# Kernel tuning notes

Hardware: AMD Instinct MI355X
Metric: run time of the kernel (lower is better)

The kernel has to match this reference:

```python
import jax, jax.numpy as jnp
import numpy as np

B, C_IN, C_OUT = 4, 64, 64
Z = H = W = 64
MZ = MH = MW = 16
R = 16


def setup_inputs() -> dict:
    key = jax.random.key(0)
    ks = jax.random.split(key, 12)
    p = lambda k, s: jax.random.normal(k, s, jnp.float32) * 0.02
    return {
        "x": jax.random.normal(ks[0], (B, C_IN, Z, H, W), jnp.float32),
        "U_in": p(ks[1], (C_IN, R)),
        "U_out": p(ks[2], (C_OUT, R)),
        "U_z": p(ks[3], (MZ, R)),
        "U_h": p(ks[4], (MH, R)),
        "U_w": p(ks[5], (MW, R)),
        "U_z2": p(ks[6], (MZ, R)),
        "U_h2": p(ks[7], (MH, R)),
        "core_r": p(ks[8], (R, R, R, R, R)),
        "core_i": p(ks[9], (R, R, R, R, R)),
        "core2_r": p(ks[10], (R, R, R, R, R)),
        "core2_i": p(ks[11], (R, R, R, R, R)),
    }


def _reconstruct(U_in, U_out, Uz, Uh, Uw, core):
    # Original: einsum('ir,or,zr,hr,wr,abcde->iozwh', ..., core).
    # core's a..e indices are summed independently of the shared r index,
    # so the weight equals the CP outer product scaled by core.sum().
    c = jnp.complex64
    w = jnp.einsum('ir,or,zr,hr,wr->iozwh',
                   U_in.astype(c), U_out.astype(c), Uz.astype(c),
                   Uh.astype(c), Uw.astype(c))
    return w * jnp.sum(core)  # (in, out, mz, mw, mh)


def reference(x, U_in, U_out, U_z, U_h, U_w, U_z2, U_h2,
              core_r, core_i, core2_r, core2_i):
    mz, mh, mw = U_z.shape[0], U_h.shape[0], U_w.shape[0]
    b, _, z, h, w = x.shape
    core = core_r + 1j * core_i
    core2 = core2_r + 1j * core2_i

    x_ft = jnp.fft.rfftn(x, axes=(-3, -2, -1))  # (B, Cin, Z, H, W//2+1) c64
    w1 = _reconstruct(U_in, U_out, U_z, U_h, U_w, core)
    w2 = _reconstruct(U_in, U_out, U_z2, U_h2, U_w, core2)

    lo = jnp.einsum('bixyz,ioxyz->boxyz', x_ft[:, :, :mz, :mh, :mw], w1)
    hi = jnp.einsum('bixyz,ioxyz->boxyz', x_ft[:, :, -mz:, :mh, :mw], w2)

    out_ft = jnp.zeros((b, U_out.shape[0], z, h, w // 2 + 1), jnp.complex64)
    out_ft = out_ft.at[:, :, :mz, :mh, :mw].set(lo)
    out_ft = out_ft.at[:, :, -mz:, :mh, :mw].set(hi)

    return jnp.fft.irfftn(out_ft, s=(z, h, w), axes=(-3, -2, -1)).astype(jnp.float32)
```

## Files before the change

kernel.cpp:

```cpp
#include <hip/hip_runtime.h>

#define TWOPI 6.28318530717958647692f

typedef float fvec4 __attribute__((ext_vector_type(4)));

constexpr float COSQ[17] = {
  1.0f, 0.995184727f, 0.980785280f, 0.956940336f, 0.923879533f,
  0.881921264f, 0.831469612f, 0.773010453f, 0.707106781f,
  0.634393284f, 0.555570233f, 0.471396737f, 0.382683432f,
  0.290284677f, 0.195090322f, 0.098017140f, 0.0f
};
__host__ __device__ constexpr float cos64f(int k) {
  k &= 63;
  return (k <= 16) ? COSQ[k] : (k < 32) ? -COSQ[32 - k]
       : (k <= 48) ? -COSQ[k - 32] : COSQ[64 - k];
}
__host__ __device__ constexpr float sin64f(int k) { return cos64f(k + 48); }


__global__ __launch_bounds__(256) void k_fwd_wh_core(
    const float* __restrict__ x, float2* __restrict__ A2,
    const float* __restrict__ a0, const float* __restrict__ a1,
    const float* __restrict__ a2, const float* __restrict__ a3,
    float* __restrict__ partial) {
  __shared__ float2 T[4][64][16];
  if (blockIdx.x < 256) {
    float* red = (float*)T;
    int bx = blockIdx.x & 63, by = blockIdx.x >> 6;
    const float* p = by == 0 ? a0 : by == 1 ? a1 : by == 2 ? a2 : a3;
    const fvec4* p4 = (const fvec4*)p;
    float s = 0.f;
    int base = bx * 4096 + threadIdx.x;
    #pragma unroll
    for (int i = 0; i < 16; ++i) {
      fvec4 v = __builtin_nontemporal_load(&p4[base + i * 256]);
      s += (v.x + v.y) + (v.z + v.w);
    }
    red[threadIdx.x] = s;
    __syncthreads();
    for (int off = 128; off; off >>= 1) {
      if (threadIdx.x < off) red[threadIdx.x] += red[threadIdx.x + off];
      __syncthreads();
    }
    if (threadIdx.x == 0) partial[by * 64 + bx] = red[0];
    return;
  }
  int wave = threadIdx.x >> 6, lane = threadIdx.x & 63;
  int plane = (blockIdx.x - 256) * 4 + wave;
  const float* xp = x + (size_t)plane * 4096 + lane;
  float cre[16], cim[16];
  {
    float x0 = xp[0], x32 = xp[32 * 64];
    #pragma unroll
    for (int hf = 0; hf < 16; ++hf) {
      cre[hf] = x0 + ((hf & 1) ? -x32 : x32);
      cim[hf] = 0.f;
    }
  }
  #pragma unroll
  for (int h = 1; h < 32; ++h) {
    float va = xp[h * 64], vb = xp[(64 - h) * 64];
    float u = va + vb, d = va - vb;
    #pragma unroll
    for (int hf = 0; hf < 16; ++hf) {
      cre[hf] = fmaf(u, cos64f(h * hf), cre[hf]);
      cim[hf] = fmaf(d, -sin64f(h * hf), cim[hf]);
    }
  }
  {
    int sw = lane & 15;
    #pragma unroll
    for (int hf = 0; hf < 16; ++hf)
      T[wave][lane][hf ^ sw] = make_float2(cre[hf], cim[hf]);
  }
  int hf = lane & 15, wq = lane >> 4;
  float2 rot[4], CS[4], acc[4];
  float2 T0 = T[wave][0][hf], T32 = T[wave][32][hf];
  #pragma unroll
  for (int j = 0; j < 4; ++j) {
    float c = (wq == 0) ? cos64f(4 * j)
            : (wq == 1) ? cos64f(4 * j + 1)
            : (wq == 2) ? cos64f(4 * j + 2) : cos64f(4 * j + 3);
    float s = (wq == 0) ? sin64f(4 * j)
            : (wq == 1) ? sin64f(4 * j + 1)
            : (wq == 2) ? sin64f(4 * j + 2) : sin64f(4 * j + 3);
    rot[j] = make_float2(c, s);
    CS[j] = make_float2(c, s);
    float sgn = ((wq + 4 * j) & 1) ? -1.f : 1.f;
    acc[j] = make_float2(T0.x + sgn * T32.x, T0.y + sgn * T32.y);
  }
  #pragma unroll
  for (int w = 1; w < 32; ++w) {
    float2 a = T[wave][w][hf ^ (w & 15)];
    float2 b2 = T[wave][64 - w][hf ^ ((64 - w) & 15)];
    float Sr = a.x + b2.x, Si = a.y + b2.y;
    float Dr = a.x - b2.x, Di = a.y - b2.y;
    #pragma unroll
    for (int j = 0; j < 4; ++j) {
      float C = CS[j].x, Sn = CS[j].y;
      acc[j].x = fmaf(Sr, C, fmaf(Di, Sn, acc[j].x));
      acc[j].y = fmaf(Si, C, fmaf(-Dr, Sn, acc[j].y));
      float nC = C * rot[j].x - Sn * rot[j].y;
      CS[j].y = fmaf(C, rot[j].y, Sn * rot[j].x);
      CS[j].x = nC;
    }
  }
  float2* dst = A2 + (size_t)plane * 256 + lane;
  #pragma unroll
  for (int j = 0; j < 4; ++j) dst[j * 64] = acc[j];
}

__global__ __launch_bounds__(256) void k_proj(const float2* __restrict__ A2,
                                              float2* __restrict__ P,
                                              const float* __restrict__ U_in,
                                              const float* __restrict__ partial,
                                              float* __restrict__ S) {
  if (blockIdx.x == 0 && blockIdx.y == 0 && threadIdx.x < 4) {
    float s = 0.f;
    for (int j = 0; j < 64; ++j) s += partial[threadIdx.x * 64 + j];
    S[threadIdx.x] = s;
  }
  __shared__ float sU[1024];
  int t = threadIdx.x;
  #pragma unroll
  for (int i = 0; i < 4; ++i) sU[t + 256 * i] = U_in[t + 256 * i];
  __syncthreads();
  int b = blockIdx.x >> 6, z = blockIdx.x & 63, r0 = blockIdx.y * 8;
  const float2* src = A2 + (((size_t)b * 64) * 64 + z) * 256 + t;
  float2 acc[8];
  #pragma unroll
  for (int r = 0; r < 8; ++r) acc[r] = make_float2(0.f, 0.f);
  for (int c = 0; c < 64; ++c) {
    float2 v = src[(size_t)c * 16384];
    #pragma unroll
    for (int r = 0; r < 8; ++r) {
      float u = sU[c * 16 + r0 + r];
      acc[r].x = fmaf(v.x, u, acc[r].x);
      acc[r].y = fmaf(v.y, u, acc[r].y);
    }
  }
  float2* dst = P + (((size_t)b * 16 + r0) * 64 + z) * 256 + t;
  #pragma unroll
  for (int r = 0; r < 8; ++r) dst[(size_t)r * 16384] = acc[r];
}

template <int Y>
__device__ __forceinline__ void inv_z_q(const float* __restrict__ gr,
                                        const float* __restrict__ gi,
                                        float2* __restrict__ dst) {
  if (Y == 0) {
    float sr = 0.f, si = 0.f;
    #pragma unroll
    for (int k = 0; k < 32; ++k) { sr += gr[k]; si += gi[k]; }
    dst[0] = make_float2(sr, si);
  }
  if (Y == 2) {
    float sr = 0.f, si = 0.f;
    #pragma unroll
    for (int k = 0; k < 32; ++k) {
      if (k & 1) { sr -= gr[k]; si -= gi[k]; }
      else       { sr += gr[k]; si += gi[k]; }
    }
    dst[32 * 256] = make_float2(sr, si);
  }
  constexpr int z0 = (Y == 0) ? 1 : (Y == 1) ? 9 : (Y == 2) ? 17 : 25;
  constexpr int z1 = (Y == 0) ? 8 : (Y == 1) ? 16 : (Y == 2) ? 24 : 31;
  #pragma unroll
  for (int z = z0; z <= z1; ++z) {
    float Ar = 0.f, Ai = 0.f, Br = 0.f, Bi = 0.f;
    #pragma unroll
    for (int k = 0; k < 32; ++k) {
      const int f = (k < 16) ? k : (k + 32);
      const float c = cos64f(z * f), s = sin64f(z * f);
      Ar = fmaf(gr[k], c, Ar); Ai = fmaf(gi[k], c, Ai);
      Br = fmaf(gr[k], s, Br); Bi = fmaf(gi[k], s, Bi);
    }
    dst[z * 256] = make_float2(Ar - Bi, Ai + Br);
    dst[(64 - z) * 256] = make_float2(Ar + Bi, Ai - Br);
  }
}

__global__ __launch_bounds__(256) void k_zmix(
    const float2* __restrict__ P, float2* __restrict__ Q,
    const float* __restrict__ U_z, const float* __restrict__ U_h,
    const float* __restrict__ U_w, const float* __restrict__ U_z2,
    const float* __restrict__ U_h2, const float* __restrict__ S4) {
  int br = blockIdx.x, r = br & 15, t = threadIdx.x;
  int hf = t & 15, wf = ((t >> 4) & 3) + 4 * (t >> 6);
  const float2* src = P + (size_t)br * 16384 + t;
  float2 acc[32];
  {
    float2 v0 = src[0], v32 = src[32 * 256];
    #pragma unroll
    for (int k = 0; k < 16; ++k) {
      float sgn = (k & 1) ? -1.f : 1.f;
      float2 e = make_float2(v0.x + sgn * v32.x, v0.y + sgn * v32.y);
      acc[k] = e;
      acc[k + 16] = e;
    }
  }
  #pragma unroll
  for (int z = 1; z < 32; ++z) {
    float2 a = src[z * 256], b = src[(64 - z) * 256];
    float Sr = a.x + b.x, Si = a.y + b.y;
    float Dr = a.x - b.x, Di = a.y - b.y;
    #pragma unroll
    for (int k = 0; k < 16; ++k) {
      {
        const float c = cos64f(z * k), s = sin64f(z * k);
        acc[k].x = fmaf(Sr, c, fmaf(Di, s, acc[k].x));
        acc[k].y = fmaf(Si, c, fmaf(-Dr, s, acc[k].y));
      }
      {
        const float c = cos64f(z * (k + 48)), s = sin64f(z * (k + 48));
        acc[k + 16].x = fmaf(Sr, c, fmaf(Di, s, acc[k + 16].x));
        acc[k + 16].y = fmaf(Si, c, fmaf(-Dr, s, acc[k + 16].y));
      }
    }
  }
  const float invN = 1.0f / 262144.0f;
  float S1r = S4[0] * invN, S1i = S4[1] * invN;
  float S2r = S4[2] * invN, S2i = S4[3] * invN;
  float cw = U_w[hf * 16 + r];
  float ch1 = U_h[wf * 16 + r] * cw, ch2 = U_h2[wf * 16 + r] * cw;
  float gr[32], gi[32];
  #pragma unroll
  for (int k = 0; k < 16; ++k) {
    float2 v = acc[k];
    float g = U_z[k * 16 + r] * ch1;
    float Fr = S1r * g, Fi = S1i * g;
    gr[k] = v.x * Fr - v.y * Fi;
    gi[k] = v.x * Fi + v.y * Fr;
  }
  #pragma unroll
  for (int k = 0; k < 16; ++k) {
    float2 v = acc[k + 16];
    float g = U_z2[k * 16 + r] * ch2;
    float Fr = S2r * g, Fi = S2i * g;
    gr[k + 16] = v.x * Fr - v.y * Fi;
    gi[k + 16] = v.x * Fi + v.y * Fr;
  }
  float2* dst = Q + (size_t)br * 16384 + t;
  switch (blockIdx.y) {
    case 0: inv_z_q<0>(gr, gi, dst); break;
    case 1: inv_z_q<1>(gr, gi, dst); break;
    case 2: inv_z_q<2>(gr, gi, dst); break;
    default: inv_z_q<3>(gr, gi, dst); break;
  }
}

__global__ __launch_bounds__(256) void k_inv_hw_ex(
    const float2* __restrict__ Q, float* __restrict__ out,
    const float* __restrict__ U_out) {
  __shared__ float2 sQ[16][256];
  __shared__ float2 GLo[4][256];
  int t = threadIdx.x;
  int b = blockIdx.x >> 6, z = blockIdx.x & 63, og = blockIdx.y;
  #pragma unroll
  for (int r = 0; r < 16; ++r)
    sQ[r][t] = Q[((size_t)(b * 16 + r) * 64 + z) * 256 + t];
  __syncthreads();
  int wave = t >> 6, lane = t & 63;
  float2 E2[16];
  {
    float s, c;
    sincosf((TWOPI / 64.f) * (float)lane, &s, &c);
    float2 E = make_float2(c, s);
    float2 St = E;
    #pragma unroll
    for (int wfi = 1; wfi < 16; ++wfi) {
      E2[wfi] = make_float2(E.x + E.x, E.y + E.y);
      float ex = E.x * St.x - E.y * St.y;
      E.y = fmaf(E.x, St.y, E.y * St.x);
      E.x = ex;
    }
  }
  for (int oi = 0; oi < 4; ++oi) {
    int o = og * 16 + wave * 4 + oi;
    float uo[16];
    #pragma unroll
    for (int r = 0; r < 16; ++r) uo[r] = U_out[o * 16 + r];
    #pragma unroll
    for (int q = 0; q < 4; ++q) {
      int tt = lane + 64 * q;
      float re = 0.f, im = 0.f;
      #pragma unroll
      for (int r = 0; r < 16; ++r) {
        float2 v = sQ[r][tt];
        re = fmaf(v.x, uo[r], re);
        im = fmaf(v.y, uo[r], im);
      }
      GLo[wave][tt] = make_float2(re, im);
    }
    float qre[16], qim[16];
    #pragma unroll
    for (int hfi = 0; hfi < 16; ++hfi) {
      float2 g0 = GLo[wave][hfi];
      float ar = g0.x, ai = g0.y;
      #pragma unroll
      for (int wfi = 1; wfi < 16; ++wfi) {
        float2 gv = GLo[wave][(wfi >> 2) * 64 + (wfi & 3) * 16 + hfi];
        ar = fmaf(gv.x, E2[wfi].x, fmaf(-gv.y, E2[wfi].y, ar));
        ai = fmaf(gv.x, E2[wfi].y, fmaf(gv.y, E2[wfi].x, ai));
      }
      qre[hfi] = ar; qim[hfi] = ai;
    }
    float* op = out + (((size_t)(b * 64 + o) * 64 + z)) * 4096 + lane;
    {
      float Pv = qre[0];
      #pragma unroll
      for (int hfi = 1; hfi < 16; ++hfi) Pv += qre[hfi];
      __builtin_nontemporal_store(Pv, op);
    }
    {
      float Pv = qre[0];
      #pragma unroll
      for (int hfi = 1; hfi < 16; ++hfi)
        Pv += (hfi & 1) ? -qre[hfi] : qre[hfi];
      __builtin_nontemporal_store(Pv, op + 32 * 64);
    }
    #pragma unroll
    for (int h = 1; h < 32; ++h) {
      float Pv = qre[0], Qv = 0.f;
      #pragma unroll
      for (int hfi = 1; hfi < 16; ++hfi) {
        Pv = fmaf(qre[hfi], cos64f(h * hfi), Pv);
        Qv = fmaf(qim[hfi], sin64f(h * hfi), Qv);
      }
      __builtin_nontemporal_store(Pv - Qv, op + h * 64);
      __builtin_nontemporal_store(Pv + Qv, op + (64 - h) * 64);
    }
  }
}

extern "C" void kernel_launch(void* const* d_in, const int* in_sizes, int n_in,
                              void* d_out, int out_size, void* d_ws,
                              size_t ws_size, hipStream_t stream) {
  const float* x    = (const float*)d_in[0];
  const float* Uin  = (const float*)d_in[1];
  const float* Uout = (const float*)d_in[2];
  const float* Uz   = (const float*)d_in[3];
  const float* Uh   = (const float*)d_in[4];
  const float* Uw   = (const float*)d_in[5];
  const float* Uz2  = (const float*)d_in[6];
  const float* Uh2  = (const float*)d_in[7];
  const float* cr   = (const float*)d_in[8];
  const float* ci   = (const float*)d_in[9];
  const float* c2r  = (const float*)d_in[10];
  const float* c2i  = (const float*)d_in[11];
  float* outp = (float*)d_out;

  char* ws = (char*)d_ws;
  float* S       = (float*)ws;
  float* partial = (float*)(ws + 256);
  float2* A2 = (float2*)(ws + 4096);
  float2* P  = (float2*)(ws + 33558528);
  float2* Q  = (float2*)(ws + 41947136);

  k_fwd_wh_core<<<4352, 256, 0, stream>>>(x, A2, cr, ci, c2r, c2i, partial);
  k_proj<<<dim3(256, 2), 256, 0, stream>>>(A2, P, Uin, partial, S);
  k_zmix<<<dim3(64, 4), 256, 0, stream>>>(P, Q, Uz, Uh, Uw, Uz2, Uh2, S);
  k_inv_hw_ex<<<dim3(256, 4), 256, 0, stream>>>(Q, outp, Uout);
}
```

Baseline: 171.0 us.

## Factor H-axis DFT into four decimated 16-point sub-DFTs with twiddle combine

Replaces the direct 64-point real DFT over H (31 symmetric pairs times 16 output frequencies) with a radix-4 decimation: four 16-point sub-DFTs over strided rows, using conjugate symmetry to compute only 9 outputs each, then combined with twiddles. This cuts the FMA count in the forward stage. It also adds a min-blocks-per-CU hint of 5 to the launch bounds, which caps register use and may cause spills given the larger set of temporaries.

```diff
diff --git a/kernel.cpp b/kernel.cpp
--- a/kernel.cpp
+++ b/kernel.cpp
@@ -18,7 +18,7 @@
 __host__ __device__ constexpr float sin64f(int k) { return cos64f(k + 48); }
 
 
-__global__ __launch_bounds__(256) void k_fwd_wh_core(
+__global__ __launch_bounds__(256, 5) void k_fwd_wh_core(
     const float* __restrict__ x, float2* __restrict__ A2,
     const float* __restrict__ a0, const float* __restrict__ a1,
     const float* __restrict__ a2, const float* __restrict__ a3,
@@ -49,22 +49,42 @@
   int plane = (blockIdx.x - 256) * 4 + wave;
   const float* xp = x + (size_t)plane * 4096 + lane;
   float cre[16], cim[16];
-  {
-    float x0 = xp[0], x32 = xp[32 * 64];
+  #pragma unroll
+  for (int s = 0; s < 4; ++s) {
+    float x0 = xp[s * 64], x32 = xp[(32 + s) * 64];
+    float u[8], d[8];
+    #pragma unroll
+    for (int q = 1; q < 8; ++q) {
+      float va = xp[(4 * q + s) * 64];
+      float vb = xp[(64 - 4 * q + s) * 64];
+      u[q] = va + vb;
+      d[q] = va - vb;
+    }
+    float yr[9], yi[9];
+    #pragma unroll
+    for (int k = 0; k <= 8; ++k) {
+      float r = x0 + ((k & 1) ? -x32 : x32);
+      float i2 = 0.f;
+      #pragma unroll
+      for (int q = 1; q < 8; ++q) {
+        r = fmaf(u[q], cos64f(4 * q * k), r);
+        i2 = fmaf(d[q], -sin64f(4 * q * k), i2);
+      }
+      yr[k] = r; yi[k] = i2;
+    }
     #pragma unroll
     for (int hf = 0; hf < 16; ++hf) {
-      cre[hf] = x0 + ((hf & 1) ? -x32 : x32);
-      cim[hf] = 0.f;
-    }
-  }
-  #pragma unroll
-  for (int h = 1; h < 32; ++h) {
-    float va = xp[h * 64], vb = xp[(64 - h) * 64];
-    float u = va + vb, d = va - vb;
-    #pragma unroll
-    for (int hf = 0; hf < 16; ++hf) {
-      cre[hf] = fmaf(u, cos64f(h * hf), cre[hf]);
-      cim[hf] = fmaf(d, -sin64f(h * hf), cim[hf]);
+      const int k = (hf <= 8) ? hf : 16 - hf;
+      float Yr = yr[k];
+      float Yi = (hf <= 8) ? yi[k] : -yi[k];
+      if (s == 0) {
+        cre[hf] = Yr;
+        cim[hf] = Yi;
+      } else {
+        const float c = cos64f(s * hf), sn = sin64f(s * hf);
+        cre[hf] = fmaf(Yr, c, fmaf(Yi, sn, cre[hf]));
+        cim[hf] = fmaf(Yi, c, fmaf(-Yr, sn, cim[hf]));
+      }
     }
   }
   {
```

Result: slower. 270.7 us (+58.4%).
